# Kernel tuning notes

Hardware: AMD Instinct MI355X
Metric: run time of the kernel (lower is better)

## Reference

```python
import jax, jax.numpy as jnp
import numpy as np

N_NODES = 100000
N_EDGES = 1600000
N_GRAPHS = 512
NFEAT = 64
HIDDEN = 128
NTARGETS = 16
TIME_DIM = 128
NLAYERS = 3  # conv1 + 2 extra convs


def setup_inputs() -> dict:
    key = jax.random.key(0)
    ks = jax.random.split(key, 12)
    x = jax.random.normal(ks[0], (N_NODES, NFEAT), dtype=jnp.float32)
    edge_index = jax.random.randint(ks[1], (2, N_EDGES), 0, N_NODES, dtype=jnp.int64)
    t_embedding = jax.random.normal(ks[2], (N_NODES, TIME_DIM), dtype=jnp.float32)
    batch = jnp.sort(jax.random.randint(ks[3], (N_NODES,), 0, N_GRAPHS, dtype=jnp.int64))
    s = lambda k, shp, fan_in: jax.random.normal(k, shp, jnp.float32) * (1.0 / np.sqrt(fan_in))
    Wt = s(ks[4], (TIME_DIM, HIDDEN), TIME_DIM)
    bt = jnp.zeros((HIDDEN,), jnp.float32)
    W1 = s(ks[5], (NFEAT, HIDDEN), NFEAT)
    b1 = jnp.zeros((HIDDEN,), jnp.float32)
    Ws = s(ks[6], (NLAYERS - 1, HIDDEN, HIDDEN), HIDDEN)
    bs = jnp.zeros((NLAYERS - 1, HIDDEN), jnp.float32)
    Wo = s(ks[7], (HIDDEN, NTARGETS), HIDDEN)
    bo = jnp.zeros((NTARGETS,), jnp.float32)
    return {"x": x, "edge_index": edge_index, "t_embedding": t_embedding,
            "batch": batch, "Wt": Wt, "bt": bt, "W1": W1, "b1": b1,
            "Ws": Ws, "bs": bs, "Wo": Wo, "bo": bo}


def _gcn_conv(h, src, dst, norm, W, b, n_nodes):
    # PyG GCNConv: h' = scatter_add(norm * (h @ W)[src] -> dst) + b
    h = h @ W                                   # [N, out]
    msg = h[src] * norm[:, None]                # [E+N, out]
    agg = jax.ops.segment_sum(msg, dst, num_segments=n_nodes)
    return agg + b


def reference(x, edge_index, t_embedding, batch, Wt, bt, W1, b1, Ws, bs, Wo, bo):
    n = x.shape[0]
    # add self-loops (static shapes)
    loop = jnp.arange(n, dtype=edge_index.dtype)
    src = jnp.concatenate([edge_index[0], loop])
    dst = jnp.concatenate([edge_index[1], loop])
    # symmetric normalization D^-1/2 (A+I) D^-1/2
    deg = jax.ops.segment_sum(jnp.ones(dst.shape[0], x.dtype), dst, num_segments=n)
    dinv = jnp.where(deg > 0, jax.lax.rsqrt(deg), 0.0)
    norm = dinv[src] * dinv[dst]                # [E+N]

    t_emb = jax.nn.relu(t_embedding @ Wt + bt)  # time_mlp
    h = jax.nn.relu(_gcn_conv(x, src, dst, norm, W1, b1, n)) + t_emb
    for i in range(Ws.shape[0]):
        h = jax.nn.relu(_gcn_conv(h, src, dst, norm, Ws[i], bs[i], n))

    # global mean pool over graphs
    gsum = jax.ops.segment_sum(h, batch, num_segments=N_GRAPHS)
    cnt = jax.ops.segment_sum(jnp.ones(n, h.dtype), batch, num_segments=N_GRAPHS)
    pooled = gsum / jnp.maximum(cnt, 1.0)[:, None]
    return pooled @ Wo + bo
```

## Files before the change

kernel.cpp:

```cpp
#include <hip/hip_runtime.h>

#define N_NODES  100000
#define N_EDGES  1600000
#define N_GRAPHS 512
#define HID      128
#define NB       782
#define NCHUNK   782
#define CHUNK    2048
#define ECAP     512

typedef unsigned int  uint;
typedef unsigned char uchar;
typedef unsigned short ushort;
typedef __attribute__((ext_vector_type(8))) short  short8;
typedef __attribute__((ext_vector_type(4))) float  f32x4;
typedef __attribute__((ext_vector_type(2))) float  f32x2;

__device__ inline float bflo(uint u) { return __uint_as_float(u << 16); }
__device__ inline float bfhi(uint u) { return __uint_as_float(u & 0xffff0000u); }
__device__ inline ushort f2bf(float f) {
    uint u = __float_as_uint(f);
    return (ushort)((u + 0x7fffu + ((u >> 16) & 1u)) >> 16);
}
__device__ inline uint pk(float a, float b) {
    return (uint)f2bf(a) | ((uint)f2bf(b) << 16);
}

__device__ inline void acc16_pk(uint4 hv, f32x2* a) {
    a[0] += __builtin_amdgcn_cvt_pk_f32_fp8((int)hv.x, false);
    a[1] += __builtin_amdgcn_cvt_pk_f32_fp8((int)hv.x, true);
    a[2] += __builtin_amdgcn_cvt_pk_f32_fp8((int)hv.y, false);
    a[3] += __builtin_amdgcn_cvt_pk_f32_fp8((int)hv.y, true);
    a[4] += __builtin_amdgcn_cvt_pk_f32_fp8((int)hv.z, false);
    a[5] += __builtin_amdgcn_cvt_pk_f32_fp8((int)hv.z, true);
    a[6] += __builtin_amdgcn_cvt_pk_f32_fp8((int)hv.w, false);
    a[7] += __builtin_amdgcn_cvt_pk_f32_fp8((int)hv.w, true);
}
__device__ inline void acc16_w(uint4 hv, float w, f32x2* a) {
    a[0] += w * __builtin_amdgcn_cvt_pk_f32_fp8((int)hv.x, false);
    a[1] += w * __builtin_amdgcn_cvt_pk_f32_fp8((int)hv.x, true);
    a[2] += w * __builtin_amdgcn_cvt_pk_f32_fp8((int)hv.y, false);
    a[3] += w * __builtin_amdgcn_cvt_pk_f32_fp8((int)hv.y, true);
    a[4] += w * __builtin_amdgcn_cvt_pk_f32_fp8((int)hv.z, false);
    a[5] += w * __builtin_amdgcn_cvt_pk_f32_fp8((int)hv.z, true);
    a[6] += w * __builtin_amdgcn_cvt_pk_f32_fp8((int)hv.w, false);
    a[7] += w * __builtin_amdgcn_cvt_pk_f32_fp8((int)hv.w, true);
}

__global__ __launch_bounds__(256)
void prep_kernel(const float* __restrict__ Wt, const float* __restrict__ W1,
                 const float* __restrict__ Ws, ushort* __restrict__ packed,
                 const int* __restrict__ batch, int* __restrict__ gstart,
                 const float* __restrict__ temb, ushort* __restrict__ tembb,
                 const int* __restrict__ dst, int* __restrict__ chunk_hist,
                 float* __restrict__ pooled) {
    __shared__ int h[NB];
    int b = blockIdx.x;
    int t = threadIdx.x;
    if (b < 224) {
        int tid = b * 256 + t;
        const float* src; int p; ushort* dstp;
        if (tid < 16384)      { src = Wt;         p = tid;         dstp = packed; }
        else if (tid < 24576) { src = W1;         p = tid - 16384; dstp = packed + 16384; }
        else if (tid < 40960) { src = Ws;         p = tid - 24576; dstp = packed + 24576; }
        else                  { src = Ws + 16384; p = tid - 40960; dstp = packed + 40960; }
        int j  = p & 7;
        int L  = (p >> 3) & 63;
        int cb = (p >> 9) & 7;
        int s  = p >> 12;
        int k  = s * 32 + (L >> 4) * 8 + j;
        int n  = cb * 16 + (L & 15);
        dstp[p] = f2bf(src[k * 128 + n]);
    } else if (b < 615) {
        int i = (b - 224) * 256 + t;
        if (i >= N_NODES) return;
        int bb = batch[i];
        int prev = (i == 0) ? -1 : batch[i - 1];
        for (int g = prev + 1; g <= bb; ++g) gstart[g] = i;
        if (i == N_NODES - 1) {
            for (int g = bb + 1; g <= N_GRAPHS; ++g) gstart[g] = N_NODES;
        }
    } else if (b < 3740) {
        long i = ((long)(b - 615) * 256 + t) * 16;
#pragma unroll
        for (int k = 0; k < 4; ++k) {
            float4 f = *(const float4*)(temb + i + k * 4);
            uint2 o; o.x = pk(f.x, f.y); o.y = pk(f.z, f.w);
            *(uint2*)(tembb + i + k * 4) = o;
        }
    } else if (b < 4522) {
        int c = b - 3740;
        for (int i = t; i < NB; i += 256) h[i] = 0;
        __syncthreads();
        const int4* d4 = (const int4*)dst;
#pragma unroll
        for (int k = 0; k < 2; ++k) {
            int i4 = c * (CHUNK / 4) + k * 256 + t;
            if (i4 < N_EDGES / 4) {
                int4 d = d4[i4];
                atomicAdd(&h[d.x >> 7], 1);
                atomicAdd(&h[d.y >> 7], 1);
                atomicAdd(&h[d.z >> 7], 1);
                atomicAdd(&h[d.w >> 7], 1);
            }
        }
        __syncthreads();
        for (int i = t; i < NB; i += 256) chunk_hist[c * NB + i] = h[i];
    } else {
        pooled[(b - 4522) * 256 + t] = 0.f;
    }
}


__global__ __launch_bounds__(256)
void scanA(const int* __restrict__ chunk_hist, int* __restrict__ cbaseT,
           int* __restrict__ btotal) {
    __shared__ int sc[256];
    int b = blockIdx.x, t = threadIdx.x;
    int v[4]; int sum = 0;
#pragma unroll
    for (int k = 0; k < 4; ++k) {
        int c = t * 4 + k;
        v[k] = (c < NCHUNK) ? chunk_hist[c * NB + b] : 0;
        sum += v[k];
    }
    sc[t] = sum;
    __syncthreads();
    for (int off = 1; off < 256; off <<= 1) {
        int x = (t >= off) ? sc[t - off] : 0;
        __syncthreads();
        sc[t] += x;
        __syncthreads();
    }
    int run = sc[t] - sum;
#pragma unroll
    for (int k = 0; k < 4; ++k) {
        int c = t * 4 + k;
        if (c < NCHUNK) cbaseT[b * NCHUNK + c] = run;
        run += v[k];
    }
    if (t == 255) btotal[b] = sc[255];
}

__global__ __launch_bounds__(256)
void scanB(const int* __restrict__ btotal, int* __restrict__ bstart,
           int* __restrict__ row_ptr) {
    __shared__ int sc[256];
    int t = threadIdx.x;
    int v[4]; int sum = 0;
#pragma unroll
    for (int k = 0; k < 4; ++k) {
        int idx = t * 4 + k;
        v[k] = (idx < NB) ? btotal[idx] : 0;
        sum += v[k];
    }
    sc[t] = sum;
    __syncthreads();
    for (int off = 1; off < 256; off <<= 1) {
        int x = (t >= off) ? sc[t - off] : 0;
        __syncthreads();
        sc[t] += x;
        __syncthreads();
    }
    int run = sc[t] - sum;
#pragma unroll
    for (int k = 0; k < 4; ++k) {
        int idx = t * 4 + k;
        if (idx < NB) bstart[idx] = run;
        run += v[k];
    }
    if (t == 0) { bstart[NB] = N_EDGES; row_ptr[N_NODES] = N_EDGES; }
}

__global__ __launch_bounds__(256)
void scatter_coarse(const int* __restrict__ src, const int* __restrict__ dst,
                    const int* __restrict__ cbaseT, const int* __restrict__ bstart,
                    uint* __restrict__ tmp) {
    __shared__ int cur[NB];
    int c = blockIdx.x, t = threadIdx.x;
    for (int i = t; i < NB; i += 256) cur[i] = cbaseT[i * NCHUNK + c] + bstart[i];
    __syncthreads();
    const int4* s4p = (const int4*)src;
    const int4* d4p = (const int4*)dst;
#pragma unroll
    for (int k = 0; k < 2; ++k) {
        int i4 = c * (CHUNK / 4) + k * 256 + t;
        if (i4 < N_EDGES / 4) {
            int4 s = s4p[i4];
            int4 d = d4p[i4];
            int p;
            p = atomicAdd(&cur[d.x >> 7], 1); tmp[p] = (uint)s.x | (((uint)(d.x & 127)) << 17);
            p = atomicAdd(&cur[d.y >> 7], 1); tmp[p] = (uint)s.y | (((uint)(d.y & 127)) << 17);
            p = atomicAdd(&cur[d.z >> 7], 1); tmp[p] = (uint)s.z | (((uint)(d.z & 127)) << 17);
            p = atomicAdd(&cur[d.w >> 7], 1); tmp[p] = (uint)s.w | (((uint)(d.w & 127)) << 17);
        }
    }
}

__global__ __launch_bounds__(256)
void csr_fine(const uint* __restrict__ tmp, const int* __restrict__ bstart,
              int* __restrict__ row_ptr, float* __restrict__ dinv,
              int* __restrict__ edge, const float* __restrict__ x,
              uchar* __restrict__ xb8) {
    __shared__ int   cnt[128];
    __shared__ float dvloc[128];
    __shared__ int   ps[128];
    int b = blockIdx.x, t = threadIdx.x;
    int node0 = b << 7;
    int ncnt = min(128, N_NODES - node0);
    int s = bstart[b], e = bstart[b + 1];
    if (t < 128) cnt[t] = 0;
    __syncthreads();
    for (int i = s + t; i < e; i += 256) atomicAdd(&cnt[tmp[i] >> 17], 1);
    __syncthreads();
    int c0 = (t < 128) ? cnt[t] : 0;
    if (t < 128) ps[t] = c0;
    __syncthreads();
    for (int off = 1; off < 128; off <<= 1) {
        int v = (t < 128 && t >= off) ? ps[t - off] : 0;
        __syncthreads();
        if (t < 128) ps[t] += v;
        __syncthreads();
    }
    if (t < 128) {
        int p0 = s + ps[t] - c0;
        float dv = rsqrtf((float)(c0 + 1));
        if (t < ncnt) { row_ptr[node0 + t] = p0; dinv[node0 + t] = dv; }
        dvloc[t] = dv;
        cnt[t] = p0;
    }
    __syncthreads();
    for (int i = s + t; i < e; i += 256) {
        uint rec = tmp[i];
        int p = atomicAdd(&cnt[rec >> 17], 1);
        edge[p] = (int)(rec & 0x1FFFFu);
    }
    for (int idx = t; idx < ncnt * 16; idx += 256) {
        int row = idx >> 4, q = idx & 15;
        float4 f = ((const float4*)(x + (size_t)(node0 + row) * 64))[q];
        float d = dvloc[row];
        int w = __builtin_amdgcn_cvt_pk_fp8_f32(f.x * d, f.y * d, 0, false);
        w     = __builtin_amdgcn_cvt_pk_fp8_f32(f.z * d, f.w * d, w, true);
        *(uint*)(xb8 + (size_t)(node0 + row) * 64 + q * 4) = (uint)w;
    }
}

template <int K, bool TEMB, bool OUT8, bool SCALEOUT, bool POOL>
__global__ __launch_bounds__(256)
void fused_conv(const void* __restrict__ Hv, const int* __restrict__ rp,
                const int* __restrict__ edge, const float* __restrict__ dinv,
                const ushort* __restrict__ Wp, const float* __restrict__ bias,
                const ushort* __restrict__ tembb, const ushort* __restrict__ Wtp,
                const float* __restrict__ bias_t, void* __restrict__ Ov,
                const int* __restrict__ batchp, float* __restrict__ pooled, int ntiles) {
    constexpr int LPR  = K / 16;
    constexpr int G    = 64 / LPR;
    constexpr int RPG  = 16 / G;
    constexpr int U    = 8;
    constexpr int LROW = 136;
    __shared__ __align__(16) ushort sA[4][16 * LROW];
    __shared__ uint sE[4][ECAP];
    const int wave = threadIdx.x >> 6;
    const int lane = threadIdx.x & 63;
    const int tile = blockIdx.x * 4 + wave;
    if (tile >= ntiles) return;
    const int row0 = tile * 16;
    const int g  = lane / LPR;
    const int fq = lane % LPR;
    ushort* myA = sA[wave];
    const uchar* H8 = (const uchar*)Hv;

    int   rpv = rp[row0 + ((lane < 17) ? lane : 16)];
    float dvv = dinv[row0 + ((lane < 16) ? lane : 15)];

    const int s0   = __shfl(rpv, 0);
    const int e15  = __shfl(rpv, 16);
    const int ecnt = e15 - s0;
    uint* sEw = sE[wave];
    for (int i = lane; i < ecnt && i < ECAP; i += 64)
        sEw[i] = ((const uint*)edge)[s0 + i];

    int rowA = g, rowB = 0;
    if constexpr (RPG == 2) {
        int r15  = lane & 15;
        int degk = __shfl(rpv, r15 + 1) - __shfl(rpv, r15);
        int key  = degk * 16 + r15;
#pragma unroll
        for (int kk = 2; kk <= 16; kk <<= 1) {
#pragma unroll
            for (int jm = kk >> 1; jm >= 1; jm >>= 1) {
                int other = __shfl_xor(key, jm);
                bool asc = ((lane & kk) == 0);
                bool keepmin = (((lane & jm) == 0) == asc);
                int mn = key < other ? key : other;
                int mx = key < other ? other : key;
                key = keepmin ? mn : mx;
            }
        }
        rowA = __shfl(key, g) & 15;
        rowB = __shfl(key, 15 - g) & 15;
    }

    auto phase1 = [&](auto eload) {
        for (int rr = 0; rr < RPG; ++rr) {
            int r = (RPG == 2) ? (rr == 0 ? rowA : rowB) : g;
            int v = row0 + r;
            int s = __shfl(rpv, r), e = __shfl(rpv, r + 1);
            f32x2 a[8];
            {
                uint4 xv = *(const uint4*)(H8 + (size_t)v * K + fq * 16);
                a[0] = __builtin_amdgcn_cvt_pk_f32_fp8((int)xv.x, false);
                a[1] = __builtin_amdgcn_cvt_pk_f32_fp8((int)xv.x, true);
                a[2] = __builtin_amdgcn_cvt_pk_f32_fp8((int)xv.y, false);
                a[3] = __builtin_amdgcn_cvt_pk_f32_fp8((int)xv.y, true);
                a[4] = __builtin_amdgcn_cvt_pk_f32_fp8((int)xv.z, false);
                a[5] = __builtin_amdgcn_cvt_pk_f32_fp8((int)xv.z, true);
                a[6] = __builtin_amdgcn_cvt_pk_f32_fp8((int)xv.w, false);
                a[7] = __builtin_amdgcn_cvt_pk_f32_fp8((int)xv.w, true);
            }
            int nfull = (e - s) / U;
            int j = s;
            for (int i = 0; i < nfull; ++i, j += U) {
                int sv[U];
#pragma unroll
                for (int u = 0; u < U; ++u) sv[u] = eload(j + u);
                uint4 hv[U];
#pragma unroll
                for (int u = 0; u < U; ++u)
                    hv[u] = *(const uint4*)(H8 + (size_t)sv[u] * K + fq * 16);
#pragma unroll
                for (int u = 0; u < U; ++u) acc16_pk(hv[u], a);
            }
            if (j < e) {
                int sv[U];
#pragma unroll
                for (int u = 0; u < U; ++u) {
                    int jv = j + u;
                    int jj = (jv < e) ? jv : e - 1;
                    sv[u] = eload(jj);
                }
                uint4 hv[U];
#pragma unroll
                for (int u = 0; u < U; ++u)
                    hv[u] = *(const uint4*)(H8 + (size_t)sv[u] * K + fq * 16);
#pragma unroll
                for (int u = 0; u < U; ++u) {
                    float w = (j + u < e) ? 1.0f : 0.0f;
                    acc16_w(hv[u], w, a);
                }
            }
            float dv = __shfl(dvv, r);
            uint4 o1, o2;
            o1.x = pk(a[0].x * dv, a[0].y * dv); o1.y = pk(a[1].x * dv, a[1].y * dv);
            o1.z = pk(a[2].x * dv, a[2].y * dv); o1.w = pk(a[3].x * dv, a[3].y * dv);
            o2.x = pk(a[4].x * dv, a[4].y * dv); o2.y = pk(a[5].x * dv, a[5].y * dv);
            o2.z = pk(a[6].x * dv, a[6].y * dv); o2.w = pk(a[7].x * dv, a[7].y * dv);
            *(uint4*)(myA + r * LROW + fq * 16)     = o1;
            *(uint4*)(myA + r * LROW + fq * 16 + 8) = o2;
        }
    };
    if (ecnt <= ECAP) {
        phase1([&](int jj) { return (int)sEw[jj - s0]; });
    } else {
        phase1([&](int jj) { return (int)((const uint*)edge)[jj]; });
    }

    const int m = lane & 15, q = lane >> 4;
    f32x4 acc[8];
#pragma unroll
    for (int cb = 0; cb < 8; ++cb) acc[cb] = {0.f, 0.f, 0.f, 0.f};
    constexpr int S = K / 32;
#pragma unroll
    for (int s = 0; s < S; ++s) {
        short8 av = *(const short8*)(myA + m * LROW + s * 32 + q * 8);
#pragma unroll
        for (int cb = 0; cb < 8; ++cb) {
            short8 b = *(const short8*)(Wp + (size_t)((s * 8 + cb) * 64 + lane) * 8);
            acc[cb] = __builtin_amdgcn_mfma_f32_16x16x32_bf16(av, b, acc[cb], 0, 0, 0);
        }
    }

    f32x4 acc2[TEMB ? 8 : 1];
    if constexpr (TEMB) {
#pragma unroll
        for (int cb = 0; cb < 8; ++cb) acc2[cb] = {0.f, 0.f, 0.f, 0.f};
        const ushort* Arow = tembb + (size_t)(row0 + m) * 128 + q * 8;
#pragma unroll
        for (int s2 = 0; s2 < 4; ++s2) {
            short8 av = *(const short8*)(Arow + s2 * 32);
#pragma unroll
            for (int cb = 0; cb < 8; ++cb) {
                short8 b = *(const short8*)(Wtp + (size_t)((s2 * 8 + cb) * 64 + lane) * 8);
                acc2[cb] = __builtin_amdgcn_mfma_f32_16x16x32_bf16(av, b, acc2[cb], 0, 0, 0);
            }
        }
    }

    float dsc[4];
    if constexpr (SCALEOUT) {
#pragma unroll
        for (int r = 0; r < 4; ++r) dsc[r] = __shfl(dvv, q * 4 + r);
    }
    if constexpr (!OUT8) {
        ushort* Ob = (ushort*)Ov;
#pragma unroll
        for (int cb = 0; cb < 8; ++cb) {
            int colc = cb * 16 + m;
            float bv = bias[colc];
            float bt2 = TEMB ? bias_t[colc] : 0.f;
#pragma unroll
            for (int r = 0; r < 4; ++r) {
                int row = q * 4 + r;
                float v = fmaxf(acc[cb][r] + bv, 0.0f);
                if (TEMB) v += fmaxf(acc2[cb][r] + bt2, 0.0f);
                if (SCALEOUT) v *= dsc[r];
                myA[row * LROW + colc] = f2bf(v);
            }
        }
        if constexpr (!POOL) {
#pragma unroll
            for (int i = 0; i < 4; ++i) {
                int srow = i * 4 + (lane >> 4);
                int scol = (lane & 15) * 8;
                *(short8*)(Ob + (size_t)(row0 + srow) * 128 + scol) =
                    *(const short8*)(myA + srow * LROW + scol);
            }
        } else {
            int gidv = (lane < 16) ? batchp[row0 + lane] : 0;
            int colb = lane * 2;
            float p0 = 0.f, p1 = 0.f;
#pragma unroll
            for (int r = 0; r < 16; ++r) {
                uint u = *(const uint*)(myA + r * LROW + colb);
                p0 += bflo(u); p1 += bfhi(u);
                int curg  = __shfl(gidv, r);
                int nextg = (r < 15) ? __shfl(gidv, r + 1) : -1;
                if (nextg != curg) {
                    atomicAdd(&pooled[curg * 128 + colb],     p0);
                    atomicAdd(&pooled[curg * 128 + colb + 1], p1);
                    p0 = 0.f; p1 = 0.f;
                }
            }
        }
    } else {
        uchar* st8 = (uchar*)myA;
        uchar* Ob = (uchar*)Ov;
#pragma unroll
        for (int cb = 0; cb < 8; ++cb) {
            int colc = cb * 16 + m;
            float bv = bias[colc];
            float bt2 = TEMB ? bias_t[colc] : 0.f;
#pragma unroll
            for (int r = 0; r < 4; ++r) {
                int row = q * 4 + r;
                float v = fmaxf(acc[cb][r] + bv, 0.0f);
                if (TEMB) v += fmaxf(acc2[cb][r] + bt2, 0.0f);
                if (SCALEOUT) v *= dsc[r];
                int enc = __builtin_amdgcn_cvt_pk_fp8_f32(v, v, 0, false);
                st8[row * 136 + colc] = (uchar)(enc & 0xff);
            }
        }
#pragma unroll
        for (int i = 0; i < 4; ++i) {
            int idx = i * 64 + lane;
            int srow = idx >> 4;
            int soff = (idx & 15) * 8;
            *(uint2*)(Ob + (size_t)(row0 + srow) * 128 + soff) =
                *(const uint2*)(st8 + srow * 136 + soff);
        }
    }
}


__global__ __launch_bounds__(256)
void head_kernel(const float* __restrict__ pooled, const int* __restrict__ gstart,
                 const float* __restrict__ Wo, const float* __restrict__ bo,
                 float* __restrict__ out) {
    int g  = blockIdx.x * 16 + (threadIdx.x >> 4);
    int tg = threadIdx.x & 15;
    if (g >= N_GRAPHS) return;
    int c = gstart[g + 1] - gstart[g];
    float inv = 1.0f / (float)(c < 1 ? 1 : c);
    float acc = bo[tg];
    for (int k = 0; k < HID; ++k)
        acc += pooled[g * 128 + k] * inv * Wo[k * 16 + tg];
    out[g * 16 + tg] = acc;
}


extern "C" void kernel_launch(void* const* d_in, const int* in_sizes, int n_in,
                              void* d_out, int out_size, void* d_ws, size_t ws_size,
                              hipStream_t stream) {
    const float* x       = (const float*)d_in[0];
    const int*   ei      = (const int*)d_in[1];
    const float* temb_in = (const float*)d_in[2];
    const int*   batch   = (const int*)d_in[3];
    const float* Wt      = (const float*)d_in[4];
    const float* bt      = (const float*)d_in[5];
    const float* W1      = (const float*)d_in[6];
    const float* b1      = (const float*)d_in[7];
    const float* Ws      = (const float*)d_in[8];
    const float* bs      = (const float*)d_in[9];
    const float* Wo      = (const float*)d_in[10];
    const float* bo      = (const float*)d_in[11];
    float* out = (float*)d_out;

    const int N = N_NODES, E = N_EDGES;
    const int* src = ei;
    const int* dst = ei + E;

    char* p = (char*)d_ws;
    auto carve = [&](size_t bytes) -> void* {
        void* r = (void*)p;
        p += (bytes + 255) & ~(size_t)255;
        return r;
    };
    int*    row_ptr    = (int*)carve((size_t)(N + 1) * 4);
    float*  dinv       = (float*)carve((size_t)N * 4);
    int*    gstart     = (int*)carve((size_t)(N_GRAPHS + 1) * 4);
    ushort* packed     = (ushort*)carve((size_t)57344 * 2);
    int*    chunk_hist = (int*)carve((size_t)NCHUNK * NB * 4);
    int*    cbaseT     = (int*)carve((size_t)NB * NCHUNK * 4);
    int*    btotal     = (int*)carve((size_t)NB * 4);
    int*    bstart     = (int*)carve((size_t)(NB + 1) * 4);
    uint*   tmp        = (uint*)carve((size_t)E * 4);
    int*    edge       = (int*)carve((size_t)E * 4);
    uchar*  xb8        = (uchar*)carve((size_t)(N + 16) * 64);
    ushort* tembb      = (ushort*)carve((size_t)N * 128 * 2);
    uchar*  H1f8       = (uchar*)carve((size_t)(N + 16) * 128);
    uchar*  H2f8       = (uchar*)carve((size_t)(N + 16) * 128);
    float*  pooled     = (float*)carve((size_t)N_GRAPHS * 128 * 4);

    const ushort* Wtp  = packed;
    const ushort* W1p  = packed + 16384;
    const ushort* Ws0p = packed + 24576;
    const ushort* Ws1p = packed + 40960;

    const int ntiles = N / 16;
    const int gblk   = (ntiles + 3) / 4;

    prep_kernel<<<4778, 256, 0, stream>>>(Wt, W1, Ws, packed, batch, gstart,
                                          temb_in, tembb, dst, chunk_hist, pooled);

    scanA<<<NB, 256, 0, stream>>>(chunk_hist, cbaseT, btotal);
    scanB<<<1, 256, 0, stream>>>(btotal, bstart, row_ptr);
    scatter_coarse<<<NCHUNK, 256, 0, stream>>>(src, dst, cbaseT, bstart, tmp);
    csr_fine<<<NB, 256, 0, stream>>>(tmp, bstart, row_ptr, dinv, edge, x, xb8);

    fused_conv<64, true, true, true, false><<<gblk, 256, 0, stream>>>(
        xb8, row_ptr, edge, dinv, W1p, b1, tembb, Wtp, bt, H1f8,
        nullptr, nullptr, ntiles);
    fused_conv<128, false, true, true, false><<<gblk, 256, 0, stream>>>(
        H1f8, row_ptr, edge, dinv, Ws0p, bs, nullptr, nullptr, nullptr, H2f8,
        nullptr, nullptr, ntiles);
    fused_conv<128, false, false, false, true><<<gblk, 256, 0, stream>>>(
        H2f8, row_ptr, edge, dinv, Ws1p, bs + 128, nullptr, nullptr, nullptr, nullptr,
        batch, pooled, ntiles);

    head_kernel<<<32, 256, 0, stream>>>(pooled, gstart, Wo, bo, out);
}
```

Before: 325.8 us.

## Halve chunk count and batch per-bucket scans with coalesced non-transposed offsets

Doubles the edge chunk size so there are half as many chunk histograms. The per-bucket prefix scan now handles 8 buckets per block and stages a chunk-by-bucket tile in shared memory, so global reads and writes use int4 loads and stores instead of strided transposed access. The scatter kernel then reads its per-chunk bases contiguously. The cost is fewer, larger blocks in the histogram and scatter kernels, with more shared-memory atomic contention per block.

Result: slower. 332.7 us (+2.1%).

```diff
diff --git a/kernel.cpp b/kernel.cpp
--- a/kernel.cpp
+++ b/kernel.cpp
@@ -5,8 +5,9 @@
 #define N_GRAPHS 512
 #define HID      128
 #define NB       782
-#define NCHUNK   782
-#define CHUNK    2048
+#define NBP      784
+#define NCHUNK   391
+#define CHUNK    4096
 #define ECAP     512
 
 typedef unsigned int  uint;
@@ -88,13 +89,13 @@
             uint2 o; o.x = pk(f.x, f.y); o.y = pk(f.z, f.w);
             *(uint2*)(tembb + i + k * 4) = o;
         }
-    } else if (b < 4522) {
+    } else if (b < 4131) {
         int c = b - 3740;
         for (int i = t; i < NB; i += 256) h[i] = 0;
         __syncthreads();
         const int4* d4 = (const int4*)dst;
 #pragma unroll
-        for (int k = 0; k < 2; ++k) {
+        for (int k = 0; k < 4; ++k) {
             int i4 = c * (CHUNK / 4) + k * 256 + t;
             if (i4 < N_EDGES / 4) {
                 int4 d = d4[i4];
@@ -105,41 +106,53 @@
             }
         }
         __syncthreads();
-        for (int i = t; i < NB; i += 256) chunk_hist[c * NB + i] = h[i];
+        for (int i = t; i < NB; i += 256) chunk_hist[c * NBP + i] = h[i];
     } else {
-        pooled[(b - 4522) * 256 + t] = 0.f;
-    }
-}
-
-
-__global__ __launch_bounds__(256)
-void scanA(const int* __restrict__ chunk_hist, int* __restrict__ cbaseT,
+        pooled[(b - 4131) * 256 + t] = 0.f;
+    }
+}
+
+
+__global__ __launch_bounds__(256)
+void scanA(const int* __restrict__ chunk_hist, int* __restrict__ cbase,
            int* __restrict__ btotal) {
+    __shared__ int hb[NCHUNK][9];
     __shared__ int sc[256];
-    int b = blockIdx.x, t = threadIdx.x;
-    int v[4]; int sum = 0;
-#pragma unroll
-    for (int k = 0; k < 4; ++k) {
-        int c = t * 4 + k;
-        v[k] = (c < NCHUNK) ? chunk_hist[c * NB + b] : 0;
-        sum += v[k];
-    }
-    sc[t] = sum;
-    __syncthreads();
-    for (int off = 1; off < 256; off <<= 1) {
-        int x = (t >= off) ? sc[t - off] : 0;
-        __syncthreads();
-        sc[t] += x;
-        __syncthreads();
-    }
-    int run = sc[t] - sum;
-#pragma unroll
-    for (int k = 0; k < 4; ++k) {
-        int c = t * 4 + k;
-        if (c < NCHUNK) cbaseT[b * NCHUNK + c] = run;
-        run += v[k];
-    }
-    if (t == 255) btotal[b] = sc[255];
+    int b0 = blockIdx.x * 8, t = threadIdx.x;
+    for (int c = t; c < NCHUNK; c += 256) {
+        int4 lo = *(const int4*)(chunk_hist + c * NBP + b0);
+        int4 hi = *(const int4*)(chunk_hist + c * NBP + b0 + 4);
+        hb[c][0] = lo.x; hb[c][1] = lo.y; hb[c][2] = lo.z; hb[c][3] = lo.w;
+        hb[c][4] = hi.x; hb[c][5] = hi.y; hb[c][6] = hi.z; hb[c][7] = hi.w;
+    }
+    __syncthreads();
+#pragma unroll 1
+    for (int j = 0; j < 8; ++j) {
+        int b = b0 + j;
+        int v0 = (2 * t     < NCHUNK) ? hb[2 * t][j]     : 0;
+        int v1 = (2 * t + 1 < NCHUNK) ? hb[2 * t + 1][j] : 0;
+        int sum = v0 + v1;
+        sc[t] = sum;
+        __syncthreads();
+        for (int off = 1; off < 256; off <<= 1) {
+            int x = (t >= off) ? sc[t - off] : 0;
+            __syncthreads();
+            sc[t] += x;
+            __syncthreads();
+        }
+        int run = sc[t] - sum;
+        if (2 * t     < NCHUNK) hb[2 * t][j]     = run;
+        if (2 * t + 1 < NCHUNK) hb[2 * t + 1][j] = run + v0;
+        if (b < NB && t == 255) btotal[b] = sc[255];
+        __syncthreads();
+    }
+    for (int c = t; c < NCHUNK; c += 256) {
+        int4 lo, hi;
+        lo.x = hb[c][0]; lo.y = hb[c][1]; lo.z = hb[c][2]; lo.w = hb[c][3];
+        hi.x = hb[c][4]; hi.y = hb[c][5]; hi.z = hb[c][6]; hi.w = hb[c][7];
+        *(int4*)(cbase + c * NBP + b0)     = lo;
+        *(int4*)(cbase + c * NBP + b0 + 4) = hi;
+    }
 }
 
 __global__ __launch_bounds__(256)
@@ -174,16 +187,16 @@
 
 __global__ __launch_bounds__(256)
 void scatter_coarse(const int* __restrict__ src, const int* __restrict__ dst,
-                    const int* __restrict__ cbaseT, const int* __restrict__ bstart,
+                    const int* __restrict__ cbase, const int* __restrict__ bstart,
                     uint* __restrict__ tmp) {
     __shared__ int cur[NB];
     int c = blockIdx.x, t = threadIdx.x;
-    for (int i = t; i < NB; i += 256) cur[i] = cbaseT[i * NCHUNK + c] + bstart[i];
+    for (int i = t; i < NB; i += 256) cur[i] = cbase[c * NBP + i] + bstart[i];
     __syncthreads();
     const int4* s4p = (const int4*)src;
     const int4* d4p = (const int4*)dst;
 #pragma unroll
-    for (int k = 0; k < 2; ++k) {
+    for (int k = 0; k < 4; ++k) {
         int i4 = c * (CHUNK / 4) + k * 256 + t;
         if (i4 < N_EDGES / 4) {
             int4 s = s4p[i4];
@@ -519,8 +532,8 @@
     float*  dinv       = (float*)carve((size_t)N * 4);
     int*    gstart     = (int*)carve((size_t)(N_GRAPHS + 1) * 4);
     ushort* packed     = (ushort*)carve((size_t)57344 * 2);
-    int*    chunk_hist = (int*)carve((size_t)NCHUNK * NB * 4);
-    int*    cbaseT     = (int*)carve((size_t)NB * NCHUNK * 4);
+    int*    chunk_hist = (int*)carve((size_t)NCHUNK * NBP * 4 + 64);
+    int*    cbase      = (int*)carve((size_t)NCHUNK * NBP * 4 + 64);
     int*    btotal     = (int*)carve((size_t)NB * 4);
     int*    bstart     = (int*)carve((size_t)(NB + 1) * 4);
     uint*   tmp        = (uint*)carve((size_t)E * 4);
@@ -539,12 +552,12 @@
     const int ntiles = N / 16;
     const int gblk   = (ntiles + 3) / 4;
 
-    prep_kernel<<<4778, 256, 0, stream>>>(Wt, W1, Ws, packed, batch, gstart,
+    prep_kernel<<<4387, 256, 0, stream>>>(Wt, W1, Ws, packed, batch, gstart,
                                           temb_in, tembb, dst, chunk_hist, pooled);
 
-    scanA<<<NB, 256, 0, stream>>>(chunk_hist, cbaseT, btotal);
+    scanA<<<(NB + 7) / 8, 256, 0, stream>>>(chunk_hist, cbase, btotal);
     scanB<<<1, 256, 0, stream>>>(btotal, bstart, row_ptr);
-    scatter_coarse<<<NCHUNK, 256, 0, stream>>>(src, dst, cbaseT, bstart, tmp);
+    scatter_coarse<<<NCHUNK, 256, 0, stream>>>(src, dst, cbase, bstart, tmp);
     csr_fine<<<NB, 256, 0, stream>>>(tmp, bstart, row_ptr, dinv, edge, x, xb8);
 
     fused_conv<64, true, true, true, false><<<gblk, 256, 0, stream>>>(
```

## Use 8-row tiles for hidden GCN layers with one row per lane group

Applied to the files above, without the earlier changes.

Makes the row tile a template parameter and launches the two 128-wide conv layers with 8-row tiles, so each lane group aggregates one destination row instead of two. This removes the in-wave bitonic degree sort and the serial two-row loop, shortening per-wave latency and doubling the wave count for the gather phase. It also adds occupancy hints to the launch bounds. The cost is that the 16-row MFMA stage now runs half empty, and per-tile overhead such as weight loads and edge staging is paid twice as often.

Result: no change. 328.5 us (+0.8%).

```diff
diff --git a/kernel.cpp b/kernel.cpp
--- a/kernel.cpp
+++ b/kernel.cpp
@@ -7,7 +7,6 @@
 #define NB       782
 #define NCHUNK   782
 #define CHUNK    2048
-#define ECAP     512
 
 typedef unsigned int  uint;
 typedef unsigned char uchar;
@@ -245,8 +244,8 @@
     }
 }
 
-template <int K, bool TEMB, bool OUT8, bool SCALEOUT, bool POOL>
-__global__ __launch_bounds__(256)
+template <int K, int TILE, int MW, bool TEMB, bool OUT8, bool SCALEOUT, bool POOL>
+__global__ __launch_bounds__(256, MW)
 void fused_conv(const void* __restrict__ Hv, const int* __restrict__ rp,
                 const int* __restrict__ edge, const float* __restrict__ dinv,
                 const ushort* __restrict__ Wp, const float* __restrict__ bias,
@@ -255,109 +254,87 @@
                 const int* __restrict__ batchp, float* __restrict__ pooled, int ntiles) {
     constexpr int LPR  = K / 16;
     constexpr int G    = 64 / LPR;
-    constexpr int RPG  = 16 / G;
+    static_assert(G >= TILE, "one row per group");
     constexpr int U    = 8;
     constexpr int LROW = 136;
+    constexpr int ECAP = (TILE == 16) ? 512 : 256;
     __shared__ __align__(16) ushort sA[4][16 * LROW];
     __shared__ uint sE[4][ECAP];
     const int wave = threadIdx.x >> 6;
     const int lane = threadIdx.x & 63;
     const int tile = blockIdx.x * 4 + wave;
     if (tile >= ntiles) return;
-    const int row0 = tile * 16;
+    const int row0 = tile * TILE;
     const int g  = lane / LPR;
     const int fq = lane % LPR;
     ushort* myA = sA[wave];
     const uchar* H8 = (const uchar*)Hv;
 
-    int   rpv = rp[row0 + ((lane < 17) ? lane : 16)];
-    float dvv = dinv[row0 + ((lane < 16) ? lane : 15)];
+    int   rpv = rp[row0 + ((lane <= TILE) ? lane : TILE)];
+    float dvv = dinv[row0 + ((lane < TILE) ? lane : TILE - 1)];
 
     const int s0   = __shfl(rpv, 0);
-    const int e15  = __shfl(rpv, 16);
-    const int ecnt = e15 - s0;
+    const int eT   = __shfl(rpv, TILE);
+    const int ecnt = eT - s0;
     uint* sEw = sE[wave];
     for (int i = lane; i < ecnt && i < ECAP; i += 64)
         sEw[i] = ((const uint*)edge)[s0 + i];
 
-    int rowA = g, rowB = 0;
-    if constexpr (RPG == 2) {
-        int r15  = lane & 15;
-        int degk = __shfl(rpv, r15 + 1) - __shfl(rpv, r15);
-        int key  = degk * 16 + r15;
-#pragma unroll
-        for (int kk = 2; kk <= 16; kk <<= 1) {
-#pragma unroll
-            for (int jm = kk >> 1; jm >= 1; jm >>= 1) {
-                int other = __shfl_xor(key, jm);
-                bool asc = ((lane & kk) == 0);
-                bool keepmin = (((lane & jm) == 0) == asc);
-                int mn = key < other ? key : other;
-                int mx = key < other ? other : key;
-                key = keepmin ? mn : mx;
-            }
-        }
-        rowA = __shfl(key, g) & 15;
-        rowB = __shfl(key, 15 - g) & 15;
-    }
-
     auto phase1 = [&](auto eload) {
-        for (int rr = 0; rr < RPG; ++rr) {
-            int r = (RPG == 2) ? (rr == 0 ? rowA : rowB) : g;
-            int v = row0 + r;
-            int s = __shfl(rpv, r), e = __shfl(rpv, r + 1);
-            f32x2 a[8];
-            {
-                uint4 xv = *(const uint4*)(H8 + (size_t)v * K + fq * 16);
-                a[0] = __builtin_amdgcn_cvt_pk_f32_fp8((int)xv.x, false);
-                a[1] = __builtin_amdgcn_cvt_pk_f32_fp8((int)xv.x, true);
-                a[2] = __builtin_amdgcn_cvt_pk_f32_fp8((int)xv.y, false);
-                a[3] = __builtin_amdgcn_cvt_pk_f32_fp8((int)xv.y, true);
-                a[4] = __builtin_amdgcn_cvt_pk_f32_fp8((int)xv.z, false);
-                a[5] = __builtin_amdgcn_cvt_pk_f32_fp8((int)xv.z, true);
-                a[6] = __builtin_amdgcn_cvt_pk_f32_fp8((int)xv.w, false);
-                a[7] = __builtin_amdgcn_cvt_pk_f32_fp8((int)xv.w, true);
-            }
-            int nfull = (e - s) / U;
-            int j = s;
-            for (int i = 0; i < nfull; ++i, j += U) {
-                int sv[U];
-#pragma unroll
-                for (int u = 0; u < U; ++u) sv[u] = eload(j + u);
-                uint4 hv[U];
-#pragma unroll
-                for (int u = 0; u < U; ++u)
-                    hv[u] = *(const uint4*)(H8 + (size_t)sv[u] * K + fq * 16);
-#pragma unroll
-                for (int u = 0; u < U; ++u) acc16_pk(hv[u], a);
-            }
-            if (j < e) {
-                int sv[U];
-#pragma unroll
-                for (int u = 0; u < U; ++u) {
-                    int jv = j + u;
-                    int jj = (jv < e) ? jv : e - 1;
-                    sv[u] = eload(jj);
-                }
-                uint4 hv[U];
-#pragma unroll
-                for (int u = 0; u < U; ++u)
-                    hv[u] = *(const uint4*)(H8 + (size_t)sv[u] * K + fq * 16);
-#pragma unroll
-                for (int u = 0; u < U; ++u) {
-                    float w = (j + u < e) ? 1.0f : 0.0f;
-                    acc16_w(hv[u], w, a);
-                }
-            }
-            float dv = __shfl(dvv, r);
-            uint4 o1, o2;
-            o1.x = pk(a[0].x * dv, a[0].y * dv); o1.y = pk(a[1].x * dv, a[1].y * dv);
-            o1.z = pk(a[2].x * dv, a[2].y * dv); o1.w = pk(a[3].x * dv, a[3].y * dv);
-            o2.x = pk(a[4].x * dv, a[4].y * dv); o2.y = pk(a[5].x * dv, a[5].y * dv);
-            o2.z = pk(a[6].x * dv, a[6].y * dv); o2.w = pk(a[7].x * dv, a[7].y * dv);
-            *(uint4*)(myA + r * LROW + fq * 16)     = o1;
-            *(uint4*)(myA + r * LROW + fq * 16 + 8) = o2;
-        }
+        int r = (g < TILE) ? g : TILE - 1;
+        int v = row0 + r;
+        int s = __shfl(rpv, r), e = __shfl(rpv, r + 1);
+        f32x2 a[8];
+        {
+            uint4 xv = *(const uint4*)(H8 + (size_t)v * K + fq * 16);
+            a[0] = __builtin_amdgcn_cvt_pk_f32_fp8((int)xv.x, false);
+            a[1] = __builtin_amdgcn_cvt_pk_f32_fp8((int)xv.x, true);
+            a[2] = __builtin_amdgcn_cvt_pk_f32_fp8((int)xv.y, false);
+            a[3] = __builtin_amdgcn_cvt_pk_f32_fp8((int)xv.y, true);
+            a[4] = __builtin_amdgcn_cvt_pk_f32_fp8((int)xv.z, false);
+            a[5] = __builtin_amdgcn_cvt_pk_f32_fp8((int)xv.z, true);
+            a[6] = __builtin_amdgcn_cvt_pk_f32_fp8((int)xv.w, false);
+            a[7] = __builtin_amdgcn_cvt_pk_f32_fp8((int)xv.w, true);
+        }
+        int nfull = (e - s) / U;
+        int j = s;
+        for (int i = 0; i < nfull; ++i, j += U) {
+            int sv[U];
+#pragma unroll
+            for (int u = 0; u < U; ++u) sv[u] = eload(j + u);
+            uint4 hv[U];
+#pragma unroll
+            for (int u = 0; u < U; ++u)
+                hv[u] = *(const uint4*)(H8 + (size_t)sv[u] * K + fq * 16);
+#pragma unroll
+            for (int u = 0; u < U; ++u) acc16_pk(hv[u], a);
+        }
+        if (j < e) {
+            int sv[U];
+#pragma unroll
+            for (int u = 0; u < U; ++u) {
+                int jv = j + u;
+                int jj = (jv < e) ? jv : e - 1;
+                sv[u] = eload(jj);
+            }
+            uint4 hv[U];
+#pragma unroll
+            for (int u = 0; u < U; ++u)
+                hv[u] = *(const uint4*)(H8 + (size_t)sv[u] * K + fq * 16);
+#pragma unroll
+            for (int u = 0; u < U; ++u) {
+                float w = (j + u < e) ? 1.0f : 0.0f;
+                acc16_w(hv[u], w, a);
+            }
+        }
+        float dv = __shfl(dvv, r);
+        uint4 o1, o2;
+        o1.x = pk(a[0].x * dv, a[0].y * dv); o1.y = pk(a[1].x * dv, a[1].y * dv);
+        o1.z = pk(a[2].x * dv, a[2].y * dv); o1.w = pk(a[3].x * dv, a[3].y * dv);
+        o2.x = pk(a[4].x * dv, a[4].y * dv); o2.y = pk(a[5].x * dv, a[5].y * dv);
+        o2.z = pk(a[6].x * dv, a[6].y * dv); o2.w = pk(a[7].x * dv, a[7].y * dv);
+        *(uint4*)(myA + r * LROW + fq * 16)     = o1;
+        *(uint4*)(myA + r * LROW + fq * 16 + 8) = o2;
     };
     if (ecnt <= ECAP) {
         phase1([&](int jj) { return (int)sEw[jj - s0]; });
@@ -399,7 +376,10 @@
     float dsc[4];
     if constexpr (SCALEOUT) {
 #pragma unroll
-        for (int r = 0; r < 4; ++r) dsc[r] = __shfl(dvv, q * 4 + r);
+        for (int r = 0; r < 4; ++r) {
+            int rr = q * 4 + r;
+            dsc[r] = __shfl(dvv, (rr < TILE) ? rr : TILE - 1);
+        }
     }
     if constexpr (!OUT8) {
         ushort* Ob = (ushort*)Ov;
@@ -419,22 +399,22 @@
         }
         if constexpr (!POOL) {
 #pragma unroll
-            for (int i = 0; i < 4; ++i) {
+            for (int i = 0; i < TILE / 4; ++i) {
                 int srow = i * 4 + (lane >> 4);
                 int scol = (lane & 15) * 8;
                 *(short8*)(Ob + (size_t)(row0 + srow) * 128 + scol) =
                     *(const short8*)(myA + srow * LROW + scol);
             }
         } else {
-            int gidv = (lane < 16) ? batchp[row0 + lane] : 0;
+            int gidv = (lane < TILE) ? batchp[row0 + lane] : 0;
             int colb = lane * 2;
             float p0 = 0.f, p1 = 0.f;
 #pragma unroll
-            for (int r = 0; r < 16; ++r) {
+            for (int r = 0; r < TILE; ++r) {
                 uint u = *(const uint*)(myA + r * LROW + colb);
                 p0 += bflo(u); p1 += bfhi(u);
                 int curg  = __shfl(gidv, r);
-                int nextg = (r < 15) ? __shfl(gidv, r + 1) : -1;
+                int nextg = (r < TILE - 1) ? __shfl(gidv, r + 1) : -1;
                 if (nextg != curg) {
                     atomicAdd(&pooled[curg * 128 + colb],     p0);
                     atomicAdd(&pooled[curg * 128 + colb + 1], p1);
@@ -461,7 +441,7 @@
             }
         }
 #pragma unroll
-        for (int i = 0; i < 4; ++i) {
+        for (int i = 0; i < TILE / 4; ++i) {
             int idx = i * 64 + lane;
             int srow = idx >> 4;
             int soff = (idx & 15) * 8;
@@ -536,8 +516,10 @@
     const ushort* Ws0p = packed + 24576;
     const ushort* Ws1p = packed + 40960;
 
-    const int ntiles = N / 16;
-    const int gblk   = (ntiles + 3) / 4;
+    const int nt16  = N / 16;
+    const int gblk1 = (nt16 + 3) / 4;
+    const int nt8   = N / 8;
+    const int gblk2 = (nt8 + 3) / 4;
 
     prep_kernel<<<4778, 256, 0, stream>>>(Wt, W1, Ws, packed, batch, gstart,
                                           temb_in, tembb, dst, chunk_hist, pooled);
@@ -547,15 +529,15 @@
     scatter_coarse<<<NCHUNK, 256, 0, stream>>>(src, dst, cbaseT, bstart, tmp);
     csr_fine<<<NB, 256, 0, stream>>>(tmp, bstart, row_ptr, dinv, edge, x, xb8);
 
-    fused_conv<64, true, true, true, false><<<gblk, 256, 0, stream>>>(
+    fused_conv<64, 16, 6, true, true, true, false><<<gblk1, 256, 0, stream>>>(
         xb8, row_ptr, edge, dinv, W1p, b1, tembb, Wtp, bt, H1f8,
-        nullptr, nullptr, ntiles);
-    fused_conv<128, false, true, true, false><<<gblk, 256, 0, stream>>>(
+        nullptr, nullptr, nt16);
+    fused_conv<128, 8, 7, false, true, true, false><<<gblk2, 256, 0, stream>>>(
         H1f8, row_ptr, edge, dinv, Ws0p, bs, nullptr, nullptr, nullptr, H2f8,
-        nullptr, nullptr, ntiles);
-    fused_conv<128, false, false, false, true><<<gblk, 256, 0, stream>>>(
+        nullptr, nullptr, nt8);
+    fused_conv<128, 8, 7, false, false, false, true><<<gblk2, 256, 0, stream>>>(
         H2f8, row_ptr, edge, dinv, Ws1p, bs + 128, nullptr, nullptr, nullptr, nullptr,
-        batch, pooled, ntiles);
+        batch, pooled, nt8);
 
     head_kernel<<<32, 256, 0, stream>>>(pooled, gstart, Wo, bo, out);
 }
```
